# Kernel tuning notes

Measured on AMD Instinct MI355X. Metric: run time of the kernel, lower is better.

The kernel has to match this reference:

```python
import jax, jax.numpy as jnp
import numpy as np

B, S, E2, E = 2, 512, 512, 256  # batch, seq, 2*encode_size, encode_size


def setup_inputs() -> dict:
    key = jax.random.key(0)
    k1, k2, k3, k4 = jax.random.split(key, 4)
    query = jax.random.normal(k1, (B, S, E2), dtype=jnp.float32)
    value = jax.random.normal(k2, (B, S, E2), dtype=jnp.float32)
    # nn.Linear weights (no bias); stored as [in, out] for x @ W convention
    Wd = jax.random.normal(k3, (E2, E), dtype=jnp.float32) * (1.0 / np.sqrt(E2))
    vd = jax.random.normal(k4, (E,), dtype=jnp.float32) * (1.0 / np.sqrt(E))
    return {"query": query, "value": value, "Wd": Wd, "vd": vd}


def reference(query, value, Wd, vd):
    # q = query.unsqueeze(1) -> [B,1,S,2E]; k = query.unsqueeze(2) -> [B,S,1,2E]
    # NOTE: original module ignores its `key` arg; both factors come from query.
    qk = query[:, None, :, :] * query[:, :, None, :]        # [B,S,S,2E]
    h = jnp.tanh(jnp.einsum('bsth,hd->bstd', qk, Wd))        # [B,S,S,E]
    sjt = jnp.einsum('bstd,d->bst', h, vd)                   # [B,S,S]
    atten = jax.nn.softmax(sjt, axis=2)                      # softmax over dim=2
    # dropout p=0.0 -> identity
    context = jnp.einsum('bst,btd->bsd', atten, value)       # bmm
    return (context, atten)
```

## Files before the change

### kernel.cpp

```cpp
#include <hip/hip_runtime.h>

#define B_  2
#define S_  512
#define E2_ 512
#define E_  256

#define TT  128
#define KB  32
#define LDK 40

using f32x4 = __attribute__((ext_vector_type(4))) float;
using f16x8 = __attribute__((ext_vector_type(8))) _Float16;

__device__ __forceinline__ float tanh_fast(float x) {
    float e = __expf(2.0f * x);
    return 1.0f - 2.0f / (e + 1.0f);
}

#define SBAR() __builtin_amdgcn_sched_barrier(0)

__global__ void prep_qh(const float* __restrict__ q, _Float16* __restrict__ qh) {
    int idx = blockIdx.x * 256 + threadIdx.x;
    float4 v = *(const float4*)(q + idx * 4);
    _Float16 h[4] = {(_Float16)v.x, (_Float16)v.y, (_Float16)v.z, (_Float16)v.w};
    *(short4*)(qh + idx * 4) = *(short4*)h;
}

__global__ void prep_w(const float* __restrict__ Wd, _Float16* __restrict__ Wp2) {
    int idx = blockIdx.x * 256 + threadIdx.x;
    int h = idx >> 8;
    int d = idx & 255;
    int ko = h >> 5;
    int kk = h & 31;
    Wp2[ko * (E_ * KB) + d * KB + kk] = (_Float16)Wd[idx];
}

__global__ __launch_bounds__(512, 4)
void stage1(const _Float16* __restrict__ qh,
            const _Float16* __restrict__ Wp2,
            const float* __restrict__ vd,
            float* __restrict__ logits ) {
    const int p  = blockIdx.x >> 7;
    const int sl = blockIdx.x & 127;
    const int b  = blockIdx.y;
    const int sj = (p >= 6) ? 3 : (p >= 3) ? 2 : (p >= 1) ? 1 : 0;
    const int ti = p - ((sj * (sj + 1)) >> 1);
    const int s  = sj * TT + sl;
    const int t0 = ti * TT;

    __shared__ _Float16 sA[2][TT * LDK];
    __shared__ _Float16 sQsh[E2_];
    __shared__ float sVd[E_];

    const int tid = threadIdx.x;
    {
        sQsh[tid] = qh[((size_t)(b * S_ + s)) * E2_ + tid];
        if (tid < E_) sVd[tid] = vd[tid];
    }
    __syncthreads();

    const int wave = tid >> 6;
    const int lane = tid & 63;
    const int wt   = wave >> 2;
    const int wd   = wave & 3;
    const int l15  = lane & 15;
    const int l4   = lane >> 4;

    const int a_row = tid >> 2;
    const int a_g   = tid & 3;
    const int a_off = a_row * LDK + a_g * 8;
    const _Float16* qt = qh + ((size_t)(b * S_ + t0 + a_row)) * E2_ + a_g * 8;

    const _Float16* wpb = Wp2 + (wd * 64 + l15) * KB + l4 * 8;

    f16x8 ra;
    auto ALOAD  = [&](int k0) { ra = *(const f16x8*)(qt + k0); };
    auto AWRITE = [&](int h)  { *(f16x8*)&sA[h][a_off] = ra; };

    f32x4 acc[4][4] = {};

    ALOAD(0);
    SBAR();
    AWRITE(0);
    SBAR();
    ALOAD(KB);
    SBAR();
    asm volatile("s_waitcnt lgkmcnt(0)" ::: "memory");
    __builtin_amdgcn_s_barrier();
    SBAR();

    for (int ko = 0; ko < E2_ / KB; ++ko) {
        const int h = ko & 1;
        const int k0 = ko * KB;
        f16x8 bf[4];
        {
            const _Float16* wk = wpb + ko * (E_ * KB);
#pragma unroll
            for (int fd = 0; fd < 4; ++fd)
                bf[fd] = *(const f16x8*)(wk + fd * 16 * KB);
        }
        SBAR();
        f16x8 af[4];
#pragma unroll
        for (int ft = 0; ft < 4; ++ft) {
            int row = wt * 64 + ft * 16 + l15;
            af[ft] = *(const f16x8*)&sA[h][row * LDK + l4 * 8];
        }
        f16x8 qsv = *(const f16x8*)&sQsh[k0 + l4 * 8];
        SBAR();
        if (ko < 15) { AWRITE(h ^ 1); SBAR(); }
        if (ko < 14) { ALOAD((ko + 2) * KB); SBAR(); }
        if (ko < 15) {
            asm volatile("s_waitcnt lgkmcnt(0)" ::: "memory");
            __builtin_amdgcn_s_barrier();
            SBAR();
        }
        f16x8 pa[4];
#pragma unroll
        for (int ft = 0; ft < 4; ++ft) pa[ft] = af[ft] * qsv;
        __builtin_amdgcn_s_setprio(1);
#pragma unroll
        for (int ft = 0; ft < 4; ++ft)
#pragma unroll
            for (int fd = 0; fd < 4; ++fd)
                acc[ft][fd] = __builtin_amdgcn_mfma_f32_16x16x32_f16(pa[ft], bf[fd], acc[ft][fd], 0, 0, 0);
        __builtin_amdgcn_s_setprio(0);
    }

    __syncthreads();

    float* sRed = (float*)&sA[0][0];
    {
        float vdr[4];
#pragma unroll
        for (int fd = 0; fd < 4; ++fd) vdr[fd] = sVd[wd * 64 + fd * 16 + l15];
#pragma unroll
        for (int ft = 0; ft < 4; ++ft) {
#pragma unroll
            for (int r = 0; r < 4; ++r) {
                float pp = 0.f;
#pragma unroll
                for (int fd = 0; fd < 4; ++fd)
                    pp += tanh_fast(acc[ft][fd][r]) * vdr[fd];
                pp += __shfl_xor(pp, 1);
                pp += __shfl_xor(pp, 2);
                pp += __shfl_xor(pp, 4);
                pp += __shfl_xor(pp, 8);
                if (l15 == 0) {
                    int tl = wt * 64 + ft * 16 + l4 * 4 + r;
                    sRed[tl * 4 + wd] = pp;
                }
            }
        }
    }
    __syncthreads();
    if (tid < TT) {
        float v = sRed[tid * 4 + 0] + sRed[tid * 4 + 1] + sRed[tid * 4 + 2] + sRed[tid * 4 + 3];
        int t = t0 + tid;
        logits[((size_t)(b * S_ + s)) * S_ + t] = v;
        logits[((size_t)(b * S_ + t)) * S_ + s] = v;
    }
}

__global__ void softmax_k(float* __restrict__ atten) {
    const int row  = blockIdx.x;
    const int lane = threadIdx.x;
    float* p = atten + (size_t)row * S_;
    float4 v0 = *(float4*)(p + lane * 8);
    float4 v1 = *(float4*)(p + lane * 8 + 4);
    float vv[8] = {v0.x, v0.y, v0.z, v0.w, v1.x, v1.y, v1.z, v1.w};
    float m = vv[0];
#pragma unroll
    for (int j = 1; j < 8; ++j) m = fmaxf(m, vv[j]);
#pragma unroll
    for (int off = 1; off < 64; off <<= 1) m = fmaxf(m, __shfl_xor(m, off));
    float ssum = 0.f;
#pragma unroll
    for (int j = 0; j < 8; ++j) { vv[j] = __expf(vv[j] - m); ssum += vv[j]; }
#pragma unroll
    for (int off = 1; off < 64; off <<= 1) ssum += __shfl_xor(ssum, off);
    float inv = 1.0f / ssum;
    float4 o0 = {vv[0] * inv, vv[1] * inv, vv[2] * inv, vv[3] * inv};
    float4 o1 = {vv[4] * inv, vv[5] * inv, vv[6] * inv, vv[7] * inv};
    *(float4*)(p + lane * 8)     = o0;
    *(float4*)(p + lane * 8 + 4) = o1;
}

__global__ __launch_bounds__(256)
void context_k(const float* __restrict__ atten, const float* __restrict__ value,
               float* __restrict__ ctx) {
    __shared__ float sA[32][65];
    __shared__ float sV[64][65];
    const int b  = blockIdx.z;
    const int s0 = blockIdx.y * 32;
    const int e0 = blockIdx.x * 64;
    const int tid = threadIdx.x;
    const int ts = tid >> 4;
    const int te = tid & 15;

    float acc[2][4] = {};
    for (int k0 = 0; k0 < S_; k0 += 64) {
        {
            int r = tid >> 3;
            int c = (tid & 7) * 8;
            const float* ga = atten + ((size_t)(b * S_ + s0 + r)) * S_ + k0 + c;
            *(float4*)&sA[r][c]     = *(const float4*)ga;
            *(float4*)&sA[r][c + 4] = *(const float4*)(ga + 4);
        }
        {
            int r = tid >> 2;
            int c = (tid & 3) * 16;
            const float* gv = value + ((size_t)(b * S_ + k0 + r)) * E2_ + e0 + c;
#pragma unroll
            for (int j = 0; j < 16; j += 4)
                *(float4*)&sV[r][c + j] = *(const float4*)(gv + j);
        }
        __syncthreads();
#pragma unroll 8
        for (int kk = 0; kk < 64; ++kk) {
            float a0 = sA[ts * 2 + 0][kk];
            float a1 = sA[ts * 2 + 1][kk];
#pragma unroll
            for (int j = 0; j < 4; ++j) {
                float vvv = sV[kk][te * 4 + j];
                acc[0][j] += a0 * vvv;
                acc[1][j] += a1 * vvv;
            }
        }
        __syncthreads();
    }
#pragma unroll
    for (int i = 0; i < 2; ++i)
#pragma unroll
        for (int j = 0; j < 4; ++j)
            ctx[((size_t)(b * S_ + s0 + ts * 2 + i)) * E2_ + e0 + te * 4 + j] = acc[i][j];
}

extern "C" void kernel_launch(void* const* d_in, const int* in_sizes, int n_in,
                              void* d_out, int out_size, void* d_ws, size_t ws_size,
                              hipStream_t stream) {
    const float* query = (const float*)d_in[0];
    const float* value = (const float*)d_in[1];
    const float* Wd    = (const float*)d_in[2];
    const float* vd    = (const float*)d_in[3];

    float* out   = (float*)d_out;
    float* ctx   = out;
    float* atten = out + (size_t)B_ * S_ * E2_;

    const size_t need = (size_t)(B_ * S_ * E2_ + 16 * E_ * KB) * sizeof(_Float16);
    _Float16* qh;
    if (ws_size >= need) {
        qh = (_Float16*)d_ws;
    } else {
        qh = (_Float16*)ctx;
    }
    _Float16* wp2 = qh + (size_t)B_ * S_ * E2_;

    prep_qh<<<dim3(512), dim3(256), 0, stream>>>(query, qh);
    prep_w<<<dim3(512), dim3(256), 0, stream>>>(Wd, wp2);
    stage1<<<dim3(1280, B_), dim3(512), 0, stream>>>(qh, wp2, vd, atten);
    softmax_k<<<dim3(B_ * S_), dim3(64), 0, stream>>>(atten);
    context_k<<<dim3(E2_ / 64, S_ / 32, B_), dim3(256), 0, stream>>>(atten, value, ctx);
}
```

Baseline: 159.0 us.

## Halve triangular tile size to 64 and fuse fp16 prep kernels

The stage-1 tile over t shrinks from 128 to 64 rows, and each block drops from 512 to 256 threads (4 waves, each owning a d-slice). The triangular schedule now covers 36 tile pairs instead of 10, so fewer redundant pairs are computed on diagonal tiles and more, smaller blocks are available to fill the GPU. The two fp16 conversion kernels for query and Wd are merged into one launch. In exchange, each block reuses the W operand across fewer rows, which increases W traffic per unit of work.

Result: faster. 145.0 us (-8.8%).

```diff
diff --git a/kernel.cpp b/kernel.cpp
--- a/kernel.cpp
+++ b/kernel.cpp
@@ -5,7 +5,7 @@
 #define E2_ 512
 #define E_  256
 
-#define TT  128
+#define TT  64
 #define KB  32
 #define LDK 40
 
@@ -19,15 +19,12 @@
 
 #define SBAR() __builtin_amdgcn_sched_barrier(0)
 
-__global__ void prep_qh(const float* __restrict__ q, _Float16* __restrict__ qh) {
+__global__ void prep_all(const float* __restrict__ q, _Float16* __restrict__ qh,
+                         const float* __restrict__ Wd, _Float16* __restrict__ Wp2) {
     int idx = blockIdx.x * 256 + threadIdx.x;
     float4 v = *(const float4*)(q + idx * 4);
-    _Float16 h[4] = {(_Float16)v.x, (_Float16)v.y, (_Float16)v.z, (_Float16)v.w};
-    *(short4*)(qh + idx * 4) = *(short4*)h;
-}
-
-__global__ void prep_w(const float* __restrict__ Wd, _Float16* __restrict__ Wp2) {
-    int idx = blockIdx.x * 256 + threadIdx.x;
+    _Float16 h4[4] = {(_Float16)v.x, (_Float16)v.y, (_Float16)v.z, (_Float16)v.w};
+    *(short4*)(qh + idx * 4) = *(short4*)h4;
     int h = idx >> 8;
     int d = idx & 255;
     int ko = h >> 5;
@@ -35,16 +32,18 @@
     Wp2[ko * (E_ * KB) + d * KB + kk] = (_Float16)Wd[idx];
 }
 
-__global__ __launch_bounds__(512, 4)
+__global__ __launch_bounds__(256, 4)
 void stage1(const _Float16* __restrict__ qh,
             const _Float16* __restrict__ Wp2,
             const float* __restrict__ vd,
             float* __restrict__ logits ) {
-    const int p  = blockIdx.x >> 7;
-    const int sl = blockIdx.x & 127;
+    const int x  = blockIdx.x;
+    const int p  = x >> 6;
+    const int sl = x & 63;
     const int b  = blockIdx.y;
-    const int sj = (p >= 6) ? 3 : (p >= 3) ? 2 : (p >= 1) ? 1 : 0;
-    const int ti = p - ((sj * (sj + 1)) >> 1);
+    int sj = 0;
+    while ((sj + 1) * (sj + 2) / 2 <= p) ++sj;
+    const int ti = p - sj * (sj + 1) / 2;
     const int s  = sj * TT + sl;
     const int t0 = ti * TT;
 
@@ -54,15 +53,16 @@
 
     const int tid = threadIdx.x;
     {
-        sQsh[tid] = qh[((size_t)(b * S_ + s)) * E2_ + tid];
-        if (tid < E_) sVd[tid] = vd[tid];
+        const _Float16* qsrow = qh + ((size_t)(b * S_ + s)) * E2_;
+        sQsh[tid]       = qsrow[tid];
+        sQsh[tid + 256] = qsrow[tid + 256];
+        sVd[tid & 255]  = vd[tid & 255];
     }
     __syncthreads();
 
     const int wave = tid >> 6;
     const int lane = tid & 63;
-    const int wt   = wave >> 2;
-    const int wd   = wave & 3;
+    const int wd   = wave;
     const int l15  = lane & 15;
     const int l4   = lane >> 4;
 
@@ -103,7 +103,7 @@
         f16x8 af[4];
 #pragma unroll
         for (int ft = 0; ft < 4; ++ft) {
-            int row = wt * 64 + ft * 16 + l15;
+            int row = ft * 16 + l15;
             af[ft] = *(const f16x8*)&sA[h][row * LDK + l4 * 8];
         }
         f16x8 qsv = *(const f16x8*)&sQsh[k0 + l4 * 8];
@@ -147,7 +147,7 @@
                 pp += __shfl_xor(pp, 4);
                 pp += __shfl_xor(pp, 8);
                 if (l15 == 0) {
-                    int tl = wt * 64 + ft * 16 + l4 * 4 + r;
+                    int tl = ft * 16 + l4 * 4 + r;
                     sRed[tl * 4 + wd] = pp;
                 }
             }
@@ -257,9 +257,8 @@
     }
     _Float16* wp2 = qh + (size_t)B_ * S_ * E2_;
 
-    prep_qh<<<dim3(512), dim3(256), 0, stream>>>(query, qh);
-    prep_w<<<dim3(512), dim3(256), 0, stream>>>(Wd, wp2);
-    stage1<<<dim3(1280, B_), dim3(512), 0, stream>>>(qh, wp2, vd, atten);
+    prep_all<<<dim3(512), dim3(256), 0, stream>>>(query, qh, Wd, wp2);
+    stage1<<<dim3(2304, B_), dim3(256), 0, stream>>>(qh, wp2, vd, atten);
     softmax_k<<<dim3(B_ * S_), dim3(64), 0, stream>>>(atten);
     context_k<<<dim3(E2_ / 64, S_ / 32, B_), dim3(256), 0, stream>>>(atten, value, ctx);
 }
```
